# Kernel tuning notes

Hardware: AMD Instinct MI355X
Metric: run time of the kernel (lower is better)

## Reference

```python
import jax, jax.numpy as jnp
import numpy as np
import math

D_MODEL = 1024
NUM_HEADS = 16
D_K = 64
B, T = 2, 2048


def setup_inputs() -> dict:
    key = jax.random.key(0)
    ks = jax.random.split(key, 12)
    s = 0.02
    return {
        "Q": jax.random.normal(ks[0], (B, T, D_MODEL), jnp.float32),
        "K": jax.random.normal(ks[1], (B, T, D_MODEL), jnp.float32),
        "V": jax.random.normal(ks[2], (B, T, D_MODEL), jnp.float32),
        # stacked per-head projection weights: [H, d_model, d_k]
        "Wq": jax.random.normal(ks[3], (NUM_HEADS, D_MODEL, D_K), jnp.float32) * s,
        "bq": jax.random.normal(ks[4], (NUM_HEADS, D_K), jnp.float32) * s,
        "Wk": jax.random.normal(ks[5], (NUM_HEADS, D_MODEL, D_K), jnp.float32) * s,
        "bk": jax.random.normal(ks[6], (NUM_HEADS, D_K), jnp.float32) * s,
        "Wv": jax.random.normal(ks[7], (NUM_HEADS, D_MODEL, D_K), jnp.float32) * s,
        "bv": jax.random.normal(ks[8], (NUM_HEADS, D_K), jnp.float32) * s,
        "Wo": jax.random.normal(ks[9], (D_MODEL, D_MODEL), jnp.float32) * s,
        "bo": jax.random.normal(ks[10], (D_MODEL,), jnp.float32) * s,
    }


def reference(Q, K, V, Wq, bq, Wk, bk, Wv, bv, Wo, bo):
    scale = 1.0 / math.sqrt(D_K)
    # fused batched per-head projections (replaces the Python per-head loop)
    Qh = jnp.einsum("btd,hdk->bhtk", Q, Wq) + bq[None, :, None, :]
    Kh = jnp.einsum("btd,hdk->bhtk", K, Wk) + bk[None, :, None, :]
    Vh = jnp.einsum("btd,hdk->bhtk", V, Wv) + bv[None, :, None, :]
    scores = jnp.einsum("bhtk,bhsk->bhts", Qh, Kh) * scale  # [B,H,T,T]
    attn = jax.nn.softmax(scores, axis=-1)
    ctx = jnp.einsum("bhts,bhsk->bhtk", attn, Vh)  # [B,H,T,d_k]
    # Faithful to the original: plain view of contiguous [B,H,T,d] into
    # [B,T,H*d] WITHOUT transposing head/time (matches torch .view semantics).
    bsz, nt = Q.shape[0], Q.shape[1]
    x = ctx.reshape(bsz, nt, NUM_HEADS * D_K)
    out = x @ Wo.T + bo
    # dropout with p=0.0 is identity; omitted for determinism
    return out
```

## Files before the change

kernel.cpp:

```cpp
#include <hip/hip_runtime.h>
#include <stdint.h>

typedef __attribute__((ext_vector_type(8))) short short8;
typedef __attribute__((ext_vector_type(4))) short short4v;
typedef __attribute__((ext_vector_type(4))) float float4v;

#define MFMA16(a, b, c) __builtin_amdgcn_mfma_f32_16x16x32_bf16((a), (b), (c), 0, 0, 0)

__device__ __forceinline__ ushort f2bf_rne(float f) {
  union { float f; unsigned u; } x; x.f = f;
  unsigned r = x.u + 0x7FFFu + ((x.u >> 16) & 1u);
  return (ushort)(r >> 16);
}
__device__ __forceinline__ ushort f2bf_trunc(float f) {
  union { float f; unsigned u; } x; x.f = f;
  return (ushort)(x.u >> 16);
}
__device__ __forceinline__ void gload16(const ushort* g, ushort* lds) {
  __builtin_amdgcn_global_load_lds(
      (__attribute__((address_space(1))) unsigned int*)g,
      (__attribute__((address_space(3))) unsigned int*)lds, 16, 0, 0);
}

#define CEXP 0.1803368801111204f

__device__ __forceinline__ void transpose64f(const float* __restrict__ in, int is,
                                             ushort* __restrict__ out, int os,
                                             ushort* lds ) {
  const int t = threadIdx.x;
#pragma unroll
  for (int it = 0; it < 2; ++it) {
    int e = it * 2048 + t * 8;
    int r = e >> 6, c = e & 63;
    const float* p = in + (size_t)r * is + c;
    float4 x0 = *(const float4*)p;
    float4 x1 = *(const float4*)(p + 4);
    ushort tv[8] __attribute__((aligned(16))) = {
        f2bf_rne(x0.x), f2bf_rne(x0.y), f2bf_rne(x0.z), f2bf_rne(x0.w),
        f2bf_rne(x1.x), f2bf_rne(x1.y), f2bf_rne(x1.z), f2bf_rne(x1.w)};
    *(uint4*)&lds[r * 72 + c] = *(const uint4*)tv;
  }
  __syncthreads();
  const int cc = t >> 2;
  const int rg = (t & 3) * 16;
  ushort tmp[16] __attribute__((aligned(16)));
#pragma unroll
  for (int i = 0; i < 16; ++i) tmp[i] = lds[(rg + i) * 72 + cc];
  *(uint4*)&out[(size_t)cc * os + rg] = *(const uint4*)&tmp[0];
  *(uint4*)&out[(size_t)cc * os + rg + 8] = *(const uint4*)&tmp[8];
}

__global__ __launch_bounds__(256) void prep_kernel(
    const float* __restrict__ Q, const float* __restrict__ K,
    const float* __restrict__ V, const float* __restrict__ Wo,
    const float* __restrict__ Wq, const float* __restrict__ Wk,
    const float* __restrict__ Wv, ushort* __restrict__ Qb, ushort* __restrict__ Kb,
    ushort* __restrict__ Vb, ushort* __restrict__ WoB, ushort* __restrict__ BtQ,
    ushort* __restrict__ BtK, ushort* __restrict__ BtV) {
  __shared__ ushort lds[64 * 72];
  const int bx = blockIdx.x;
  if (bx < 6656) {
    const float* s;
    ushort* d;
    int i;
    if (bx < 6144) {
      const int plane = bx >> 11;
      s = plane == 0 ? Q : (plane == 1 ? K : V);
      d = plane == 0 ? Qb : (plane == 1 ? Kb : Vb);
      i = ((bx & 2047) * 256 + threadIdx.x) * 8;
    } else {
      s = Wo;
      d = WoB;
      i = ((bx - 6144) * 256 + threadIdx.x) * 8;
    }
    float4 a = *(const float4*)(s + i);
    float4 b = *(const float4*)(s + i + 4);
    ushort t[8] __attribute__((aligned(16))) = {
        f2bf_rne(a.x), f2bf_rne(a.y), f2bf_rne(a.z), f2bf_rne(a.w),
        f2bf_rne(b.x), f2bf_rne(b.y), f2bf_rne(b.z), f2bf_rne(b.w)};
    *(uint4*)(d + i) = *(const uint4*)t;
  } else {
    const int rb = bx - 6656;
    const int dt = rb & 15, h = (rb >> 4) & 15, z = rb >> 8;
    const float* W = z == 0 ? Wq : (z == 1 ? Wk : Wv);
    ushort* Bt = z == 0 ? BtQ : (z == 1 ? BtK : BtV);
    transpose64f(W + h * 65536 + dt * 4096, 64, Bt + h * 65536 + dt * 64, 1024, lds);
  }
}

__global__ __launch_bounds__(256, 2) void repack_w_kernel(
    const float* __restrict__ Wq, const float* __restrict__ Wk,
    const float* __restrict__ Wv, ushort* __restrict__ BtQ, ushort* __restrict__ BtK,
    ushort* __restrict__ BtV) {
  __shared__ ushort lds[64 * 72];
  const float* W = blockIdx.z == 0 ? Wq : (blockIdx.z == 1 ? Wk : Wv);
  ushort* Bt = blockIdx.z == 0 ? BtQ : (blockIdx.z == 1 ? BtK : BtV);
  const int h = blockIdx.y, dt = blockIdx.x;
  transpose64f(W + h * 65536 + dt * 4096, 64, Bt + h * 65536 + dt * 64, 1024, lds);
}

template <int F32>
__device__ __forceinline__ void stage16(const void* G, size_t eoff, ushort* ldst) {
  if (F32) {
    const float* p = (const float*)G + eoff;
    float4 x0 = *(const float4*)p;
    float4 x1 = *(const float4*)(p + 4);
    ushort t[8] __attribute__((aligned(16))) = {
        f2bf_rne(x0.x), f2bf_rne(x0.y), f2bf_rne(x0.z), f2bf_rne(x0.w),
        f2bf_rne(x1.x), f2bf_rne(x1.y), f2bf_rne(x1.z), f2bf_rne(x1.w)};
    *(uint4*)ldst = *(const uint4*)t;
  } else {
    gload16((const ushort*)G + eoff, ldst);
  }
}

template <int AF32, int BF32>
__device__ __forceinline__ void gemm_body_basic(const void* __restrict__ A,
                                                const void* __restrict__ Bt,
                                                const float* __restrict__ bias,
                                                void* __restrict__ C, int cmode,
                                                float ascale, int N, int K, ushort* lA,
                                                ushort* lB) {
  const int tid = threadIdx.x;
  const int l = tid & 63, lane15 = l & 15, quad = l >> 4;
  const int mbase = blockIdx.y * 128, nbase = blockIdx.x * 128;
  const int w = tid >> 6;
  const int wrow = (w >> 1) * 64, wcol = (w & 1) * 64;
  const int e0 = tid * 8;
  const int e1 = 2048 + tid * 8;
  const int r0 = e0 >> 5, c0 = e0 & 31;
  const int r1 = e1 >> 5, c1 = e1 & 31;

  float4v acc[4][4];
#pragma unroll
  for (int i = 0; i < 4; ++i)
#pragma unroll
    for (int j = 0; j < 4; ++j) acc[i][j] = (float4v){0.f, 0.f, 0.f, 0.f};

  for (int kb = 0; kb < K; kb += 32) {
    __syncthreads();
    stage16<AF32>(A, (size_t)(mbase + r0) * K + c0 + kb, &lA[e0]);
    stage16<AF32>(A, (size_t)(mbase + r1) * K + c1 + kb, &lA[e1]);
    stage16<BF32>(Bt, (size_t)(nbase + r0) * K + c0 + kb, &lB[e0]);
    stage16<BF32>(Bt, (size_t)(nbase + r1) * K + c1 + kb, &lB[e1]);
    asm volatile("s_waitcnt vmcnt(0)" ::: "memory");
    __syncthreads();
    short8 a[4], b[4];
#pragma unroll
    for (int i = 0; i < 4; ++i) {
      a[i] = *(const short8*)&lA[(wrow + i * 16 + lane15) * 32 + quad * 8];
      b[i] = *(const short8*)&lB[(wcol + i * 16 + lane15) * 32 + quad * 8];
    }
#pragma unroll
    for (int i = 0; i < 4; ++i)
#pragma unroll
      for (int j = 0; j < 4; ++j) acc[i][j] = MFMA16(a[i], b[j], acc[i][j]);
  }

  if (cmode == 3) {
    __syncthreads();
    uint* sp = (uint*)lA + w * 576;
    const int bb = mbase >> 11;
    const int tb = (mbase & 2047) + wrow;
#pragma unroll
    for (int j = 0; j < 4; ++j) {
      {
        const int n = nbase + wcol + j * 16 + lane15;
        const float bvs = bias[n];
#pragma unroll
        for (int i = 0; i < 4; ++i)
#pragma unroll
          for (int rp = 0; rp < 2; ++rp) {
            const uint lo = f2bf_rne((acc[i][j][2 * rp] + bvs) * ascale);
            const uint hi = f2bf_rne((acc[i][j][2 * rp + 1] + bvs) * ascale);
            sp[36 * lane15 + i * 8 + quad * 2 + rp] = lo | (hi << 16);
          }
      }
#pragma unroll
      for (int t = 0; t < 2; ++t) {
        const int row = t * 8 + (l >> 3);
        const int c = l & 7;
        uint4 d = *(const uint4*)(sp + 36 * row + 4 * c);
        const int ng = nbase + wcol + j * 16 + row;
        ushort* dst = (ushort*)C + ((size_t)(bb * 1024 + ng)) * 2048 + tb + c * 8;
        *(uint4*)dst = d;
      }
    }
    return;
  }

#pragma unroll
  for (int j = 0; j < 4; ++j) {
    const int n = nbase + wcol + j * 16 + lane15;
    const float bvs = bias[n];
#pragma unroll
    for (int i = 0; i < 4; ++i) {
      const int m0 = mbase + wrow + i * 16 + quad * 4;
#pragma unroll
      for (int r = 0; r < 4; ++r) {
        const float val = (acc[i][j][r] + bvs) * ascale;
        if (cmode == 1) {
          const int m = m0 + r;
          const int bb = m >> 11, t = m & 2047;
          ((ushort*)C)[((size_t)(bb * 1024 + n)) * 2048 + t] = f2bf_rne(val);
        } else if (cmode == 2) {
          ((float*)C)[(size_t)(m0 + r) * N + n] = val;
        } else {
          ((ushort*)C)[(size_t)(m0 + r) * N + n] = f2bf_rne(val);
        }
      }
    }
  }
}

__global__ __launch_bounds__(256, 2) void proj3_kernel(
    const ushort* __restrict__ Qb, const ushort* __restrict__ Kb,
    const ushort* __restrict__ Vb, const ushort* __restrict__ BtQ,
    const ushort* __restrict__ BtK, const ushort* __restrict__ BtV,
    const float* __restrict__ bq, const float* __restrict__ bk,
    const float* __restrict__ bv, ushort* __restrict__ Qh, ushort* __restrict__ Kh,
    ushort* __restrict__ Vt) {
  __shared__ ushort lA[5120], lB[4096];
  if (blockIdx.z == 0)
    gemm_body_basic<0, 0>(Qb, BtQ, bq, Qh, 0, CEXP, 1024, 1024, lA, lB);
  else if (blockIdx.z == 1)
    gemm_body_basic<0, 0>(Kb, BtK, bk, Kh, 0, 1.0f, 1024, 1024, lA, lB);
  else
    gemm_body_basic<0, 0>(Vb, BtV, bv, Vt, 3, 1.0f, 1024, 1024, lA, lB);
}

__global__ __launch_bounds__(256, 2) void gemm_out_kernel(
    const ushort* __restrict__ X, const ushort* __restrict__ WoB,
    const float* __restrict__ bo, float* __restrict__ out) {
  __shared__ ushort lA[4096], lB[2048];
  const int tid = threadIdx.x;
  const int l = tid & 63, lane15 = l & 15, quad = l >> 4;
  const int mbase = blockIdx.y * 128, nbase = blockIdx.x * 64;
  const int wv = tid >> 6;
  const int wrow = wv * 32;
  const int e0 = tid * 8;
  const int e1 = 2048 + tid * 8;
  const int r0 = e0 >> 5, c0 = e0 & 31;
  const int r1 = e1 >> 5, c1 = e1 & 31;
  const ushort* Ag0 = X + (size_t)(mbase + r0) * 1024 + c0;
  const ushort* Ag1 = X + (size_t)(mbase + r1) * 1024 + c1;
  const ushort* Bg0 = WoB + (size_t)(nbase + r0) * 1024 + c0;

  float4v acc[2][4];
#pragma unroll
  for (int i = 0; i < 2; ++i)
#pragma unroll
    for (int j = 0; j < 4; ++j) acc[i][j] = (float4v){0.f, 0.f, 0.f, 0.f};

  for (int kb = 0; kb < 1024; kb += 32) {
    __syncthreads();
    gload16(Ag0 + kb, &lA[e0]);
    gload16(Ag1 + kb, &lA[e1]);
    gload16(Bg0 + kb, &lB[e0]);
    asm volatile("s_waitcnt vmcnt(0)" ::: "memory");
    __syncthreads();
    short8 a[2], b[4];
#pragma unroll
    for (int i = 0; i < 2; ++i)
      a[i] = *(const short8*)&lA[(wrow + i * 16 + lane15) * 32 + quad * 8];
#pragma unroll
    for (int j = 0; j < 4; ++j)
      b[j] = *(const short8*)&lB[(j * 16 + lane15) * 32 + quad * 8];
#pragma unroll
    for (int i = 0; i < 2; ++i)
#pragma unroll
      for (int j = 0; j < 4; ++j) acc[i][j] = MFMA16(a[i], b[j], acc[i][j]);
  }

#pragma unroll
  for (int j = 0; j < 4; ++j) {
    const int n = nbase + j * 16 + lane15;
    const float bvs = bo[n];
#pragma unroll
    for (int i = 0; i < 2; ++i) {
      const int m0 = mbase + wrow + i * 16 + quad * 4;
#pragma unroll
      for (int r = 0; r < 4; ++r) out[(size_t)(m0 + r) * 1024 + n] = acc[i][j][r] + bvs;
    }
  }
}

__global__ __launch_bounds__(256, 2) void proj3f_kernel(
    const float* __restrict__ Q, const float* __restrict__ Kin,
    const float* __restrict__ V, const ushort* __restrict__ BtQ,
    const ushort* __restrict__ BtK, const ushort* __restrict__ BtV,
    const float* __restrict__ bq, const float* __restrict__ bk,
    const float* __restrict__ bv, ushort* __restrict__ Qh, ushort* __restrict__ Kh,
    ushort* __restrict__ Vt) {
  __shared__ ushort lA[5120], lB[4096];
  if (blockIdx.z == 0)
    gemm_body_basic<1, 0>(Q, BtQ, bq, Qh, 0, CEXP, 1024, 1024, lA, lB);
  else if (blockIdx.z == 1)
    gemm_body_basic<1, 0>(Kin, BtK, bk, Kh, 0, 1.0f, 1024, 1024, lA, lB);
  else
    gemm_body_basic<1, 0>(V, BtV, bv, Vt, 3, 1.0f, 1024, 1024, lA, lB);
}

__global__ __launch_bounds__(256, 2) void gemm_btf_kernel(
    const ushort* __restrict__ X, const float* __restrict__ Wo,
    const float* __restrict__ bo, float* __restrict__ out) {
  __shared__ ushort lA[5120], lB[4096];
  gemm_body_basic<0, 1>(X, Wo, bo, out, 2, 1.0f, 1024, 1024, lA, lB);
}

__global__ __launch_bounds__(512, 4) void attn_kernel(const ushort* __restrict__ Qh,
                                                      const ushort* __restrict__ Kh,
                                                      const ushort* __restrict__ Vt,
                                                      ushort* __restrict__ ctxout) {
  __shared__ ushort lK[64 * 64];
  __shared__ ushort lV[64 * 64];
  __shared__ ushort pl_all[8][16 * 68];
  const int tid = threadIdx.x, l = tid & 63, wv = tid >> 6;
  const int lane15 = l & 15, quad = l >> 4;
  const int bh = blockIdx.x, b = bh >> 4, h = bh & 15;
  const int q0 = blockIdx.y * 128 + wv * 16;

  const int sr = tid >> 3;
  const int scb = (tid & 7) ^ (sr & 7);
  const ushort* Kp = Kh + (size_t)(b * 2048) * 1024 + h * 64;
  const ushort* Vp = Vt + (size_t)(bh * 64) * 2048;
  const ushort* Kg = Kp + (size_t)sr * 1024 + scb * 8;
  const ushort* Vg = Vp + (size_t)sr * 2048 + scb * 8;
  ushort* lKd = lK + tid * 8;
  ushort* lVd = lV + tid * 8;

  const ushort* qrow = Qh + (size_t)(b * 2048 + q0 + lane15) * 1024 + h * 64;
  const short8 qa0 = *(const short8*)&qrow[quad * 8];
  const short8 qa1 = *(const short8*)&qrow[32 + quad * 8];

  const int xm = lane15 & 7;
  const int fr0 = lane15 * 64 + ((quad ^ xm) * 8);
  const int fr1 = lane15 * 64 + (((quad + 4) ^ xm) * 8);

  ushort* pl = &pl_all[wv][0];
  const short8 ones = {0x3F80, 0x3F80, 0x3F80, 0x3F80, 0x3F80, 0x3F80, 0x3F80, 0x3F80};

  float4v o[4];
  float4v lf = (float4v){0.f, 0.f, 0.f, 0.f};
#pragma unroll
  for (int i = 0; i < 4; ++i) o[i] = (float4v){0.f, 0.f, 0.f, 0.f};

  for (int s0 = 0; s0 < 2048; s0 += 64) {
    __syncthreads();
    gload16(Kg + (size_t)s0 * 1024, lKd);
    gload16(Vg + s0, lVd);
    asm volatile("s_waitcnt vmcnt(0)" ::: "memory");
    __syncthreads();

    float4v sb[4];
#pragma unroll
    for (int i = 0; i < 4; ++i) {
      short8 k0 = *(const short8*)&lK[i * 1024 + fr0];
      short8 k1 = *(const short8*)&lK[i * 1024 + fr1];
      float4v c = (float4v){0.f, 0.f, 0.f, 0.f};
      c = MFMA16(qa0, k0, c);
      c = MFMA16(qa1, k1, c);
      sb[i] = c;
    }
#pragma unroll
    for (int i = 0; i < 4; ++i)
#pragma unroll
      for (int r = 0; r < 4; ++r)
        pl[(quad * 4 + r) * 68 + i * 16 + lane15] =
            f2bf_trunc(__builtin_amdgcn_exp2f(sb[i][r]));
    short4v p0a = *(const short4v*)&pl[lane15 * 68 + quad * 8];
    short4v p0b = *(const short4v*)&pl[lane15 * 68 + quad * 8 + 4];
    short4v p1a = *(const short4v*)&pl[lane15 * 68 + 32 + quad * 8];
    short4v p1b = *(const short4v*)&pl[lane15 * 68 + 32 + quad * 8 + 4];
    short8 pa0 = __builtin_shufflevector(p0a, p0b, 0, 1, 2, 3, 4, 5, 6, 7);
    short8 pa1 = __builtin_shufflevector(p1a, p1b, 0, 1, 2, 3, 4, 5, 6, 7);
    lf = MFMA16(pa0, ones, lf);
    lf = MFMA16(pa1, ones, lf);
#pragma unroll
    for (int nf = 0; nf < 4; ++nf) {
      short8 v0 = *(const short8*)&lV[nf * 1024 + fr0];
      short8 v1 = *(const short8*)&lV[nf * 1024 + fr1];
      o[nf] = MFMA16(pa0, v0, o[nf]);
      o[nf] = MFMA16(pa1, v1, o[nf]);
    }
  }

  float inv[4];
#pragma unroll
  for (int r = 0; r < 4; ++r) inv[r] = (lf[r] > 0.f) ? 1.0f / lf[r] : 0.0f;
  ushort* crow = ctxout + ((size_t)bh * 2048 + q0) * 64;
#pragma unroll
  for (int nf = 0; nf < 4; ++nf)
#pragma unroll
    for (int r = 0; r < 4; ++r)
      crow[(size_t)(quad * 4 + r) * 64 + nf * 16 + lane15] = f2bf_rne(o[nf][r] * inv[r]);
}

extern "C" void kernel_launch(void* const* d_in, const int* in_sizes, int n_in,
                              void* d_out, int out_size, void* d_ws, size_t ws_size,
                              hipStream_t stream) {
  const float* Q = (const float*)d_in[0];
  const float* K = (const float*)d_in[1];
  const float* V = (const float*)d_in[2];
  const float* Wq = (const float*)d_in[3];
  const float* bq = (const float*)d_in[4];
  const float* Wk = (const float*)d_in[5];
  const float* bk = (const float*)d_in[6];
  const float* Wv = (const float*)d_in[7];
  const float* bv = (const float*)d_in[8];
  const float* Wo = (const float*)d_in[9];
  const float* bo = (const float*)d_in[10];
  float* out = (float*)d_out;
  ushort* ws = (ushort*)d_ws;

  if (ws_size >= (58ull << 20)) {
    ushort* Qh = ws;
    ushort* Kh = Qh + (4 << 20);
    ushort* Vt = Kh + (4 << 20);
    ushort* BtQ = Vt + (4 << 20);
    ushort* BtK = BtQ + (1 << 20);
    ushort* BtV = BtK + (1 << 20);
    ushort* X = BtQ;
    ushort* WoB = ws + (16ull << 20);
    ushort* Qb = WoB + (1 << 20);
    ushort* Kb = Qb + (4 << 20);
    ushort* Vb = Kb + (4 << 20);

    prep_kernel<<<dim3(7424), 256, 0, stream>>>(Q, K, V, Wo, Wq, Wk, Wv, Qb, Kb, Vb,
                                                WoB, BtQ, BtK, BtV);
    proj3_kernel<<<dim3(8, 32, 3), 256, 0, stream>>>(Qb, Kb, Vb, BtQ, BtK, BtV, bq, bk,
                                                     bv, Qh, Kh, Vt);
    attn_kernel<<<dim3(32, 16), 512, 0, stream>>>(Qh, Kh, Vt, X);
    gemm_out_kernel<<<dim3(16, 32), 256, 0, stream>>>(X, WoB, bo, out);
  } else {
    ushort* Qh = ws;
    ushort* Kh = Qh + (4 << 20);
    ushort* Vt = Kh + (4 << 20);
    ushort* R = Vt + (4 << 20);
    ushort* BtQ = R;
    ushort* BtK = R + (1 << 20);
    ushort* BtV = R + (2 << 20);
    ushort* X = R;

    repack_w_kernel<<<dim3(16, 16, 3), 256, 0, stream>>>(Wq, Wk, Wv, BtQ, BtK, BtV);
    proj3f_kernel<<<dim3(8, 32, 3), 256, 0, stream>>>(Q, K, V, BtQ, BtK, BtV, bq, bk, bv,
                                                      Qh, Kh, Vt);
    attn_kernel<<<dim3(32, 16), 512, 0, stream>>>(Qh, Kh, Vt, X);
    gemm_btf_kernel<<<dim3(8, 32), 256, 0, stream>>>(X, Wo, bo, out);
  }
}
```

Before: 227.2 us.

## Double-buffer K/V tiles in attention and raise MFMA wave priority

```diff
diff --git a/kernel.cpp b/kernel.cpp
--- a/kernel.cpp
+++ b/kernel.cpp
@@ -312,8 +312,8 @@
                                                       const ushort* __restrict__ Kh,
                                                       const ushort* __restrict__ Vt,
                                                       ushort* __restrict__ ctxout) {
-  __shared__ ushort lK[64 * 64];
-  __shared__ ushort lV[64 * 64];
+  __shared__ ushort lK[2][64 * 64];
+  __shared__ ushort lV[2][64 * 64];
   __shared__ ushort pl_all[8][16 * 68];
   const int tid = threadIdx.x, l = tid & 63, wv = tid >> 6;
   const int lane15 = l & 15, quad = l >> 4;
@@ -326,8 +326,6 @@
   const ushort* Vp = Vt + (size_t)(bh * 64) * 2048;
   const ushort* Kg = Kp + (size_t)sr * 1024 + scb * 8;
   const ushort* Vg = Vp + (size_t)sr * 2048 + scb * 8;
-  ushort* lKd = lK + tid * 8;
-  ushort* lVd = lV + tid * 8;
 
   const ushort* qrow = Qh + (size_t)(b * 2048 + q0 + lane15) * 1024 + h * 64;
   const short8 qa0 = *(const short8*)&qrow[quad * 8];
@@ -345,23 +343,32 @@
 #pragma unroll
   for (int i = 0; i < 4; ++i) o[i] = (float4v){0.f, 0.f, 0.f, 0.f};
 
+  gload16(Kg, &lK[0][tid * 8]);
+  gload16(Vg, &lV[0][tid * 8]);
+  asm volatile("s_waitcnt vmcnt(0)" ::: "memory");
+  __syncthreads();
+
+  int cur = 0;
   for (int s0 = 0; s0 < 2048; s0 += 64) {
-    __syncthreads();
-    gload16(Kg + (size_t)s0 * 1024, lKd);
-    gload16(Vg + s0, lVd);
-    asm volatile("s_waitcnt vmcnt(0)" ::: "memory");
-    __syncthreads();
+    if (s0 + 64 < 2048) {
+      gload16(Kg + (size_t)(s0 + 64) * 1024, &lK[cur ^ 1][tid * 8]);
+      gload16(Vg + (s0 + 64), &lV[cur ^ 1][tid * 8]);
+    }
+    const ushort* Kl = &lK[cur][0];
+    const ushort* Vl = &lV[cur][0];
 
     float4v sb[4];
+    __builtin_amdgcn_s_setprio(1);
 #pragma unroll
     for (int i = 0; i < 4; ++i) {
-      short8 k0 = *(const short8*)&lK[i * 1024 + fr0];
-      short8 k1 = *(const short8*)&lK[i * 1024 + fr1];
+      short8 k0 = *(const short8*)&Kl[i * 1024 + fr0];
+      short8 k1 = *(const short8*)&Kl[i * 1024 + fr1];
       float4v c = (float4v){0.f, 0.f, 0.f, 0.f};
       c = MFMA16(qa0, k0, c);
       c = MFMA16(qa1, k1, c);
       sb[i] = c;
     }
+    __builtin_amdgcn_s_setprio(0);
 #pragma unroll
     for (int i = 0; i < 4; ++i)
 #pragma unroll
@@ -374,15 +381,21 @@
     short4v p1b = *(const short4v*)&pl[lane15 * 68 + 32 + quad * 8 + 4];
     short8 pa0 = __builtin_shufflevector(p0a, p0b, 0, 1, 2, 3, 4, 5, 6, 7);
     short8 pa1 = __builtin_shufflevector(p1a, p1b, 0, 1, 2, 3, 4, 5, 6, 7);
+    __builtin_amdgcn_s_setprio(1);
     lf = MFMA16(pa0, ones, lf);
     lf = MFMA16(pa1, ones, lf);
 #pragma unroll
     for (int nf = 0; nf < 4; ++nf) {
-      short8 v0 = *(const short8*)&lV[nf * 1024 + fr0];
-      short8 v1 = *(const short8*)&lV[nf * 1024 + fr1];
+      short8 v0 = *(const short8*)&Vl[nf * 1024 + fr0];
+      short8 v1 = *(const short8*)&Vl[nf * 1024 + fr1];
       o[nf] = MFMA16(pa0, v0, o[nf]);
       o[nf] = MFMA16(pa1, v1, o[nf]);
     }
+    __builtin_amdgcn_s_setprio(0);
+
+    asm volatile("s_waitcnt vmcnt(0)" ::: "memory");
+    __syncthreads();
+    cur ^= 1;
   }
 
   float inv[4];
```

After: 221.3 us. 1.03x faster.
